# Kernel optimization log

Measured on AMD Instinct MI355X. Metric: run time of the kernel, lower is better.

The kernel has to match this reference:

```python
import jax, jax.numpy as jnp
import numpy as np

B, Q, KV = 2, 2048, 2048
D_MODEL = 1024
N_HEADS = 16
D_KV = 64
EPS = 1e-6


def setup_inputs() -> dict:
    key = jax.random.key(0)
    ks = jax.random.split(key, 7)
    s = 0.02
    return {
        "hidden_states": jax.random.normal(ks[0], (B, Q, D_MODEL), jnp.float32),
        "key_value_states": jax.random.normal(ks[1], (B, KV, D_MODEL), jnp.float32),
        "wq": jax.random.normal(ks[2], (D_MODEL, N_HEADS * D_KV), jnp.float32) * s,
        "wk": jax.random.normal(ks[3], (D_MODEL, N_HEADS * D_KV), jnp.float32) * s,
        "wv": jax.random.normal(ks[4], (D_MODEL, N_HEADS * D_KV), jnp.float32) * s,
        "wo": jax.random.normal(ks[5], (N_HEADS * D_KV, D_MODEL), jnp.float32) * s,
        "norm_w": jnp.ones((D_MODEL,), jnp.float32),
    }


def reference(hidden_states, key_value_states, wq, wk, wv, wo, norm_w):
    # RMSNorm (T5-style, no mean subtraction)
    var = jnp.mean(jnp.square(hidden_states), axis=-1, keepdims=True)
    normed = hidden_states * jax.lax.rsqrt(var + EPS) * norm_w

    b, q_len, _ = hidden_states.shape
    kv_len = key_value_states.shape[1]

    def split_heads(x):  # [b, s, H*d] -> [b, H, s, d]
        return x.reshape(b, -1, N_HEADS, D_KV).transpose(0, 2, 1, 3)

    q = split_heads(normed @ wq)              # [b,H,q,d]
    k = split_heads(key_value_states @ wk)    # [b,H,kv,d]
    v = split_heads(key_value_states @ wv)    # [b,H,kv,d]

    # T5 attention: NO 1/sqrt(d) scaling; position_bias is zeros here
    # (has_relative_attention_bias=False, no mask) so it is a no-op.
    scores = jnp.einsum("bhqd,bhkd->bhqk", q, k)
    attn = jax.nn.softmax(scores.astype(jnp.float32), axis=-1).astype(scores.dtype)
    ctx = jnp.einsum("bhqk,bhkd->bhqd", attn, v)
    ctx = ctx.transpose(0, 2, 1, 3).reshape(b, q_len, N_HEADS * D_KV)
    attn_out = ctx @ wo

    # residual connection
    return hidden_states + attn_out
```

## Files before the change

kernel.cpp:

```cpp
#include <hip/hip_runtime.h>


typedef __attribute__((ext_vector_type(8))) short  s16x8;
typedef __attribute__((ext_vector_type(4))) float  f32x4;
typedef __attribute__((ext_vector_type(4))) int    i32x4;

#define LOG2E 1.4426950408889634f
#define EXP2(x) __builtin_amdgcn_exp2f(x)

__device__ __forceinline__ unsigned short f2bf(float f) {
  unsigned int u = __builtin_bit_cast(unsigned int, f);
  return (unsigned short)((u + 0x7FFFu + ((u >> 16) & 1u)) >> 16);
}

__device__ __forceinline__ unsigned cvtpk(float lo, float hi) {
  unsigned r;
  asm("v_cvt_pk_bf16_f32 %0, %1, %2" : "=v"(r) : "v"(lo), "v"(hi));
  return r;
}

__device__ __forceinline__ void gload16(const void* g, void* l) {
  __builtin_amdgcn_global_load_lds(
      (const __attribute__((address_space(1))) unsigned int*)g,
      (__attribute__((address_space(3))) unsigned int*)l, 16, 0, 0);
}

__global__ __launch_bounds__(256) void k_transpose4(
    const float* __restrict__ a0, const float* __restrict__ a1,
    const float* __restrict__ a2, const float* __restrict__ a3,
    unsigned short* __restrict__ o0, unsigned short* __restrict__ o1,
    unsigned short* __restrict__ o2, unsigned short* __restrict__ o3) {
  int z = blockIdx.z;
  const float* in = (z == 0) ? a0 : (z == 1) ? a1 : (z == 2) ? a2 : a3;
  unsigned short* out = (z == 0) ? o0 : (z == 1) ? o1 : (z == 2) ? o2 : o3;
  __shared__ float tile[64][65];
  int t = threadIdx.x;
  int tx = t & 15, ty = t >> 4;
  int r0 = blockIdx.y * 64, c0 = blockIdx.x * 64;
#pragma unroll
  for (int p = 0; p < 4; ++p) {
    int r = p * 16 + ty;
    float4 v = *reinterpret_cast<const float4*>(in + (size_t)(r0 + r) * 1024 + c0 + tx * 4);
    tile[r][tx * 4 + 0] = v.x; tile[r][tx * 4 + 1] = v.y;
    tile[r][tx * 4 + 2] = v.z; tile[r][tx * 4 + 3] = v.w;
  }
  __syncthreads();
#pragma unroll
  for (int p = 0; p < 4; ++p) {
    int c = p * 16 + ty;
    unsigned int lo = (unsigned int)f2bf(tile[tx * 4 + 0][c]) |
                      ((unsigned int)f2bf(tile[tx * 4 + 1][c]) << 16);
    unsigned int hi = (unsigned int)f2bf(tile[tx * 4 + 2][c]) |
                      ((unsigned int)f2bf(tile[tx * 4 + 3][c]) << 16);
    uint2 pk2; pk2.x = lo; pk2.y = hi;
    *reinterpret_cast<uint2*>(out + (size_t)(c0 + c) * 1024 + r0 + tx * 4) = pk2;
  }
}

__global__ __launch_bounds__(256) void k_rmsnorm(
    const float* __restrict__ hs, const float* __restrict__ w,
    unsigned short* __restrict__ out) {
  int row = blockIdx.x, t = threadIdx.x;
  float4 v = *reinterpret_cast<const float4*>(hs + (size_t)row * 1024 + t * 4);
  float s = v.x * v.x + v.y * v.y + v.z * v.z + v.w * v.w;
#pragma unroll
  for (int m = 1; m < 64; m <<= 1) s += __shfl_xor(s, m);
  __shared__ float ps[4];
  if ((t & 63) == 0) ps[t >> 6] = s;
  __syncthreads();
  float tot = ps[0] + ps[1] + ps[2] + ps[3];
  float sc = rsqrtf(tot * (1.0f / 1024.0f) + 1e-6f) * LOG2E;
  float4 wv = *reinterpret_cast<const float4*>(w + t * 4);
  unsigned int lo = (unsigned int)f2bf(v.x * sc * wv.x) |
                    ((unsigned int)f2bf(v.y * sc * wv.y) << 16);
  unsigned int hi = (unsigned int)f2bf(v.z * sc * wv.z) |
                    ((unsigned int)f2bf(v.w * sc * wv.w) << 16);
  uint2 pk2; pk2.x = lo; pk2.y = hi;
  *reinterpret_cast<uint2*>(out + (size_t)row * 1024 + t * 4) = pk2;
}

__global__ __launch_bounds__(256) void k_cast(
    const float* __restrict__ in, unsigned short* __restrict__ out, int n4) {
  int i = blockIdx.x * 256 + threadIdx.x;
  int stride = gridDim.x * 256;
  for (; i < n4; i += stride) {
    float4 v = *reinterpret_cast<const float4*>(in + (size_t)i * 4);
    unsigned int lo = (unsigned int)f2bf(v.x) | ((unsigned int)f2bf(v.y) << 16);
    unsigned int hi = (unsigned int)f2bf(v.z) | ((unsigned int)f2bf(v.w) << 16);
    uint2 pk2; pk2.x = lo; pk2.y = hi;
    *reinterpret_cast<uint2*>(out + (size_t)i * 4) = pk2;
  }
}

__device__ __forceinline__ void gemm_body(
    const unsigned short* __restrict__ A, const unsigned short* __restrict__ Bt,
    void* __restrict__ Cout, const float* __restrict__ resid, int mode) {
  __shared__ __align__(16) char sm[65536];
  int t = threadIdx.x;
  int bn = blockIdx.x, bm = blockIdx.y;
  int m0 = bm * 128, n0 = bn * 128;
  int lane = t & 63, w = t >> 6, lr = lane & 15, lg = lane >> 4;
  int wr = w >> 1, wc = w & 1;

  f32x4 acc[4][4] = {};

  const char* aA = (const char*)A + ((size_t)(m0 + (t >> 3)) * 1024 + (t & 7) * 8) * 2;
  const char* aB = (const char*)Bt + ((size_t)(n0 + (t >> 3)) * 1024 + (t & 7) * 8) * 2;

  auto stage = [&](int buf, int kt) {
    int koff = kt * 128;
    char* As = sm + buf * 16384;
    char* Bs = sm + 32768 + buf * 16384;
#pragma unroll
    for (int c = 0; c < 4; ++c) {
      gload16(aA + (size_t)c * 65536 + koff, As + c * 4096 + t * 16);
      gload16(aB + (size_t)c * 65536 + koff, Bs + c * 4096 + t * 16);
    }
  };

  stage(0, 0);
  __syncthreads();
  int cur = 0;
  for (int kt = 0; kt < 16; ++kt) {
    if (kt < 15) stage(cur ^ 1, kt + 1);
    const char* As = sm + cur * 16384;
    const char* Bs = sm + 32768 + cur * 16384;
    s16x8 af[2][4], bfr[2][4];
#pragma unroll
    for (int ks = 0; ks < 2; ++ks) {
#pragma unroll
      for (int m = 0; m < 4; ++m)
        af[ks][m] = *reinterpret_cast<const s16x8*>(
            As + (wr * 64 + m * 16 + lr) * 128 + ks * 64 + lg * 16);
#pragma unroll
      for (int n = 0; n < 4; ++n)
        bfr[ks][n] = *reinterpret_cast<const s16x8*>(
            Bs + (wc * 64 + n * 16 + lr) * 128 + ks * 64 + lg * 16);
    }
#pragma unroll
    for (int ks = 0; ks < 2; ++ks)
#pragma unroll
      for (int m = 0; m < 4; ++m)
#pragma unroll
        for (int n = 0; n < 4; ++n)
          acc[m][n] = __builtin_amdgcn_mfma_f32_16x16x32_bf16(af[ks][m], bfr[ks][n], acc[m][n], 0, 0, 0);
    __syncthreads();
    cur ^= 1;
  }

#pragma unroll
  for (int m = 0; m < 4; ++m)
#pragma unroll
    for (int n = 0; n < 4; ++n) {
      int colg = n0 + wc * 64 + n * 16 + lr;
      int rowb = m0 + wr * 64 + m * 16 + lg * 4;
      if (mode == 0) {
        unsigned short* C = (unsigned short*)Cout;
#pragma unroll
        for (int r = 0; r < 4; ++r)
          C[(size_t)(rowb + r) * 1024 + colg] = f2bf(acc[m][n][r]);
      } else if (mode == 1) {
        int h = colg >> 6, d = colg & 63;
        int b = rowb >> 11, kv = rowb & 2047;
        unsigned short* C = (unsigned short*)Cout +
            ((size_t)((b * 16 + h) * 64 + d) * 2048 + kv);
        unsigned int lo = (unsigned int)f2bf(acc[m][n][0]) |
                          ((unsigned int)f2bf(acc[m][n][1]) << 16);
        unsigned int hi = (unsigned int)f2bf(acc[m][n][2]) |
                          ((unsigned int)f2bf(acc[m][n][3]) << 16);
        uint2 pk2; pk2.x = lo; pk2.y = hi;
        *reinterpret_cast<uint2*>(C) = pk2;
      } else {
        float* C = (float*)Cout;
#pragma unroll
        for (int r = 0; r < 4; ++r) {
          size_t idx = (size_t)(rowb + r) * 1024 + colg;
          C[idx] = resid[idx] + acc[m][n][r];
        }
      }
    }
}

__global__ __launch_bounds__(256) void k_gemm_qkv(
    const unsigned short* __restrict__ normed, const unsigned short* __restrict__ kvb,
    const unsigned short* __restrict__ wqT, const unsigned short* __restrict__ wkT,
    const unsigned short* __restrict__ wvT,
    unsigned short* __restrict__ qb, unsigned short* __restrict__ kb,
    unsigned short* __restrict__ vTb) {
  int z = blockIdx.z;
  const unsigned short* A = (z == 0) ? normed : kvb;
  const unsigned short* B = (z == 0) ? wqT : (z == 1) ? wkT : wvT;
  void* C = (z == 0) ? (void*)qb : (z == 1) ? (void*)kb : (void*)vTb;
  gemm_body(A, B, C, nullptr, (z == 2) ? 1 : 0);
}

__global__ __launch_bounds__(256) void k_gemm_o(
    const unsigned short* __restrict__ ctxb, const unsigned short* __restrict__ woT,
    float* __restrict__ out, const float* __restrict__ hs) {
  gemm_body(ctxb, woT, (void*)out, hs, 2);
}

__global__ __launch_bounds__(512, 4) void k_attn(
    const unsigned short* __restrict__ q, const unsigned short* __restrict__ k,
    const unsigned short* __restrict__ vt, unsigned short* __restrict__ ctx) {
  __shared__ __align__(16) char sm[65536];
  int t = threadIdx.x, w = t >> 6, lane = t & 63, lr = lane & 15, lg = lane >> 4;

  int bid = blockIdx.x;
  int xcd = bid & 7, slot = bid >> 3;
  int bh = xcd * 4 + (slot >> 4);
  int qt = slot & 15;
  int b = bh >> 4, h = bh & 15;

  const char* qB = (const char*)q + ((size_t)(b * 2048 + qt * 128) * 1024 + h * 64) * 2;
  const char* kB = (const char*)k + ((size_t)(b * 2048) * 1024 + h * 64) * 2;
  const char* vB = (const char*)vt + (size_t)bh * 64 * 4096;

  int krow = t >> 3;
  int kcb  = ((t & 7) * 16) ^ ((krow & 7) << 4);
  int vrow = t >> 4;
  int vcb  = ((t & 15) * 16) ^ ((vrow & 7) << 4);

  auto stageKV = [&](int buf, int it2) {
    char* Kd = sm + buf * 16384;
    char* Vd = sm + 32768 + buf * 16384;
    const char* kb2 = kB + (size_t)(it2 * 128) * 2048;
    const char* vb2 = vB + it2 * 256;
#pragma unroll
    for (int c = 0; c < 2; ++c) {
      gload16(kb2 + (size_t)(c * 64 + krow) * 2048 + kcb, Kd + c * 8192 + t * 16);
      gload16(vb2 + (size_t)(c * 32 + vrow) * 4096 + vcb, Vd + c * 8192 + t * 16);
    }
  };

#pragma unroll
  for (int c = 0; c < 2; ++c)
    gload16(qB + (size_t)(c * 64 + krow) * 2048 + kcb, sm + c * 8192 + t * 16);
  __syncthreads();
  s16x8 qa[2];
#pragma unroll
  for (int ks = 0; ks < 2; ++ks) {
    int row = w * 16 + lr;
    qa[ks] = *reinterpret_cast<const s16x8*>(
        sm + row * 128 + ((ks * 64 + lg * 16) ^ ((lr & 7) << 4)));
  }
  __syncthreads();
  stageKV(0, 0);
  asm volatile("s_waitcnt vmcnt(0)" ::: "memory");
  __builtin_amdgcn_s_barrier();
  __builtin_amdgcn_sched_barrier(0);

  f32x4 octx[4] = {};
  float mrun = -1e30f;
  float lsum = 0.0f;

  int cur = 0;
  for (int it = 0; it < 16; ++it) {
    if (it < 15) stageKV(cur ^ 1, it + 1);

    const char* Ks = sm + cur * 16384;
    const char* Vs = sm + 32768 + cur * 16384;

    f32x4 s2[8] = {};
#pragma unroll
    for (int ks = 0; ks < 2; ++ks) {
      s16x8 ka[8];
#pragma unroll
      for (int n = 0; n < 8; ++n)
        ka[n] = *reinterpret_cast<const s16x8*>(
            Ks + (n * 16 + lr) * 128 + ((ks * 64 + lg * 16) ^ ((lr & 7) << 4)));
#pragma unroll
      for (int n = 0; n < 8; ++n)
        s2[n] = __builtin_amdgcn_mfma_f32_16x16x32_bf16(ka[n], qa[ks], s2[n], 0, 0, 0);
    }

    float m2 = s2[0][0];
#pragma unroll
    for (int n = 0; n < 8; ++n)
#pragma unroll
      for (int r = 0; r < 4; ++r) m2 = fmaxf(m2, s2[n][r]);
    m2 = fmaxf(m2, __shfl_xor(m2, 16));
    m2 = fmaxf(m2, __shfl_xor(m2, 32));
    if (__any(m2 > mrun + 8.0f)) {
      float mx = fmaxf(mrun, m2);
      float sc = EXP2(mrun - mx);
      mrun = mx;
      lsum *= sc;
#pragma unroll
      for (int r = 0; r < 4; ++r) {
        float scr = __shfl(sc, lg * 4 + r);
#pragma unroll
        for (int nd = 0; nd < 4; ++nd) octx[nd][r] *= scr;
      }
    }

    unsigned pk[8][2];
    {
      float a0 = 0.0f, a1 = 0.0f, a2 = 0.0f, a3 = 0.0f;
#pragma unroll
      for (int n = 0; n < 8; ++n) {
        float p0 = EXP2(s2[n][0] - mrun);
        float p1 = EXP2(s2[n][1] - mrun);
        float p2 = EXP2(s2[n][2] - mrun);
        float p3 = EXP2(s2[n][3] - mrun);
        a0 += p0; a1 += p1; a2 += p2; a3 += p3;
        pk[n][0] = cvtpk(p0, p1);
        pk[n][1] = cvtpk(p2, p3);
      }
      lsum += (a0 + a1) + (a2 + a3);
    }

#pragma unroll
    for (int ks = 0; ks < 4; ++ks) {
      s16x8 vb[4];
#pragma unroll
      for (int nd = 0; nd < 4; ++nd) {
        int row = nd * 16 + lr;
        int swz = (lr & 7) << 4;
        uint2 v1 = *reinterpret_cast<const uint2*>(
            Vs + row * 256 + ((ks * 64 + lg * 8) ^ swz));
        uint2 v2 = *reinterpret_cast<const uint2*>(
            Vs + row * 256 + ((ks * 64 + 32 + lg * 8) ^ swz));
        i32x4 vv; vv[0] = (int)v1.x; vv[1] = (int)v1.y;
        vv[2] = (int)v2.x; vv[3] = (int)v2.y;
        vb[nd] = __builtin_bit_cast(s16x8, vv);
      }
      i32x4 pv;
      pv[0] = (int)pk[2 * ks][0];     pv[1] = (int)pk[2 * ks][1];
      pv[2] = (int)pk[2 * ks + 1][0]; pv[3] = (int)pk[2 * ks + 1][1];
      s16x8 pa = __builtin_bit_cast(s16x8, pv);
#pragma unroll
      for (int nd = 0; nd < 4; ++nd)
        octx[nd] = __builtin_amdgcn_mfma_f32_16x16x32_bf16(pa, vb[nd], octx[nd], 0, 0, 0);
    }

    if (it < 15) {
      asm volatile("s_waitcnt vmcnt(0)" ::: "memory");
      __builtin_amdgcn_s_barrier();
      __builtin_amdgcn_sched_barrier(0);
      cur ^= 1;
    }
  }

  {
    float tot = lsum;
    tot += __shfl_xor(tot, 16);
    tot += __shfl_xor(tot, 32);
    float inv = 1.0f / tot;
#pragma unroll
    for (int r = 0; r < 4; ++r) {
      float invr = __shfl(inv, lg * 4 + r);
      int qrow = qt * 128 + w * 16 + lg * 4 + r;
#pragma unroll
      for (int nd = 0; nd < 4; ++nd)
        ctx[(size_t)(b * 2048 + qrow) * 1024 + h * 64 + nd * 16 + lr] =
            f2bf(octx[nd][r] * invr);
    }
  }
}

extern "C" void kernel_launch(void* const* d_in, const int* in_sizes, int n_in,
                              void* d_out, int out_size, void* d_ws, size_t ws_size,
                              hipStream_t stream) {
  const float* hs  = (const float*)d_in[0];
  const float* kvs = (const float*)d_in[1];
  const float* wq  = (const float*)d_in[2];
  const float* wk  = (const float*)d_in[3];
  const float* wv  = (const float*)d_in[4];
  const float* wo  = (const float*)d_in[5];
  const float* nw  = (const float*)d_in[6];
  float* out = (float*)d_out;
  char* ws = (char*)d_ws;

  unsigned short* normed = (unsigned short*)(ws + (size_t)0);
  unsigned short* kvb    = (unsigned short*)(ws + ((size_t)8 << 20));
  unsigned short* wqT    = (unsigned short*)(ws + ((size_t)16 << 20));
  unsigned short* wkT    = (unsigned short*)(ws + ((size_t)18 << 20));
  unsigned short* wvT    = (unsigned short*)(ws + ((size_t)20 << 20));
  unsigned short* woT    = (unsigned short*)(ws + ((size_t)22 << 20));
  unsigned short* qb     = (unsigned short*)(ws + ((size_t)24 << 20));
  unsigned short* kb     = (unsigned short*)(ws + ((size_t)32 << 20));
  unsigned short* vTb    = (unsigned short*)(ws + ((size_t)40 << 20));
  unsigned short* ctxb   = (unsigned short*)(ws + ((size_t)48 << 20));

  k_transpose4<<<dim3(16, 16, 4), 256, 0, stream>>>(wq, wk, wv, wo, wqT, wkT, wvT, woT);
  k_rmsnorm<<<4096, 256, 0, stream>>>(hs, nw, normed);
  k_cast<<<1024, 256, 0, stream>>>(kvs, kvb, 1048576);

  k_gemm_qkv<<<dim3(8, 32, 3), 256, 0, stream>>>(normed, kvb, wqT, wkT, wvT, qb, kb, vTb);

  k_attn<<<512, 512, 0, stream>>>(qb, kb, vTb, ctxb);

  k_gemm_o<<<dim3(8, 32), 256, 0, stream>>>(ctxb, woT, out, hs);
}
```

Before: 141.9 us.

## Prefetch attention KV two tiles ahead, fuse prep kernels, shrink O-proj tile

The attention loop now keeps two K/V tiles in flight and waits only for the older one with a partial vmcnt. It also raises wave priority around the MFMA blocks and uses three-input max for the row max. The RMSNorm and bf16 cast kernels are merged into one launch. The GEMM body is templated on M tile and mode, so the output projection uses 64-row tiles to double its block count. The aims are to hide load latency, cut launch overhead and improve occupancy on the small O GEMM, at the risk of a wrong vmcnt count if the per-stage load count differs.

Result: slower. 169.9 us (+19.7%).

```diff
diff --git a/kernel.cpp b/kernel.cpp
--- a/kernel.cpp
+++ b/kernel.cpp
@@ -17,6 +17,10 @@
   unsigned r;
   asm("v_cvt_pk_bf16_f32 %0, %1, %2" : "=v"(r) : "v"(lo), "v"(hi));
   return r;
+}
+
+__device__ __forceinline__ float f3max(float a, float b, float c) {
+  return fmaxf(fmaxf(a, b), c);
 }
 
 __device__ __forceinline__ void gload16(const void* g, void* l) {
@@ -57,65 +61,69 @@
   }
 }
 
-__global__ __launch_bounds__(256) void k_rmsnorm(
+__global__ __launch_bounds__(256) void k_prep(
     const float* __restrict__ hs, const float* __restrict__ w,
-    unsigned short* __restrict__ out) {
-  int row = blockIdx.x, t = threadIdx.x;
-  float4 v = *reinterpret_cast<const float4*>(hs + (size_t)row * 1024 + t * 4);
-  float s = v.x * v.x + v.y * v.y + v.z * v.z + v.w * v.w;
-#pragma unroll
-  for (int m = 1; m < 64; m <<= 1) s += __shfl_xor(s, m);
-  __shared__ float ps[4];
-  if ((t & 63) == 0) ps[t >> 6] = s;
-  __syncthreads();
-  float tot = ps[0] + ps[1] + ps[2] + ps[3];
-  float sc = rsqrtf(tot * (1.0f / 1024.0f) + 1e-6f) * LOG2E;
-  float4 wv = *reinterpret_cast<const float4*>(w + t * 4);
-  unsigned int lo = (unsigned int)f2bf(v.x * sc * wv.x) |
-                    ((unsigned int)f2bf(v.y * sc * wv.y) << 16);
-  unsigned int hi = (unsigned int)f2bf(v.z * sc * wv.z) |
-                    ((unsigned int)f2bf(v.w * sc * wv.w) << 16);
-  uint2 pk2; pk2.x = lo; pk2.y = hi;
-  *reinterpret_cast<uint2*>(out + (size_t)row * 1024 + t * 4) = pk2;
-}
-
-__global__ __launch_bounds__(256) void k_cast(
-    const float* __restrict__ in, unsigned short* __restrict__ out, int n4) {
-  int i = blockIdx.x * 256 + threadIdx.x;
-  int stride = gridDim.x * 256;
-  for (; i < n4; i += stride) {
-    float4 v = *reinterpret_cast<const float4*>(in + (size_t)i * 4);
-    unsigned int lo = (unsigned int)f2bf(v.x) | ((unsigned int)f2bf(v.y) << 16);
-    unsigned int hi = (unsigned int)f2bf(v.z) | ((unsigned int)f2bf(v.w) << 16);
+    unsigned short* __restrict__ normed,
+    const float* __restrict__ kvs, unsigned short* __restrict__ kvb) {
+  int t = threadIdx.x;
+  if (blockIdx.x < 4096) {
+    int row = blockIdx.x;
+    float4 v = *reinterpret_cast<const float4*>(hs + (size_t)row * 1024 + t * 4);
+    float s = v.x * v.x + v.y * v.y + v.z * v.z + v.w * v.w;
+#pragma unroll
+    for (int m = 1; m < 64; m <<= 1) s += __shfl_xor(s, m);
+    __shared__ float ps[4];
+    if ((t & 63) == 0) ps[t >> 6] = s;
+    __syncthreads();
+    float tot = ps[0] + ps[1] + ps[2] + ps[3];
+    float sc = rsqrtf(tot * (1.0f / 1024.0f) + 1e-6f) * LOG2E;
+    float4 wv = *reinterpret_cast<const float4*>(w + t * 4);
+    unsigned int lo = (unsigned int)f2bf(v.x * sc * wv.x) |
+                      ((unsigned int)f2bf(v.y * sc * wv.y) << 16);
+    unsigned int hi = (unsigned int)f2bf(v.z * sc * wv.z) |
+                      ((unsigned int)f2bf(v.w * sc * wv.w) << 16);
     uint2 pk2; pk2.x = lo; pk2.y = hi;
-    *reinterpret_cast<uint2*>(out + (size_t)i * 4) = pk2;
-  }
-}
-
+    *reinterpret_cast<uint2*>(normed + (size_t)row * 1024 + t * 4) = pk2;
+  } else {
+    int i = (blockIdx.x - 4096) * 256 + t;
+    for (; i < 1048576; i += 1024 * 256) {
+      float4 v = *reinterpret_cast<const float4*>(kvs + (size_t)i * 4);
+      unsigned int lo = (unsigned int)f2bf(v.x) | ((unsigned int)f2bf(v.y) << 16);
+      unsigned int hi = (unsigned int)f2bf(v.z) | ((unsigned int)f2bf(v.w) << 16);
+      uint2 pk2; pk2.x = lo; pk2.y = hi;
+      *reinterpret_cast<uint2*>(kvb + (size_t)i * 4) = pk2;
+    }
+  }
+}
+
+template <int BM, int MODE>
 __device__ __forceinline__ void gemm_body(
     const unsigned short* __restrict__ A, const unsigned short* __restrict__ Bt,
-    void* __restrict__ Cout, const float* __restrict__ resid, int mode) {
-  __shared__ __align__(16) char sm[65536];
+    void* __restrict__ Cout, const float* __restrict__ resid) {
+  constexpr int MF = BM / 32;
+  constexpr int ATILE = BM * 128;
+  __shared__ __align__(16) char sm[2 * ATILE + 32768];
   int t = threadIdx.x;
   int bn = blockIdx.x, bm = blockIdx.y;
-  int m0 = bm * 128, n0 = bn * 128;
+  int m0 = bm * BM, n0 = bn * 128;
   int lane = t & 63, w = t >> 6, lr = lane & 15, lg = lane >> 4;
   int wr = w >> 1, wc = w & 1;
 
-  f32x4 acc[4][4] = {};
+  f32x4 acc[MF][4] = {};
 
   const char* aA = (const char*)A + ((size_t)(m0 + (t >> 3)) * 1024 + (t & 7) * 8) * 2;
   const char* aB = (const char*)Bt + ((size_t)(n0 + (t >> 3)) * 1024 + (t & 7) * 8) * 2;
 
   auto stage = [&](int buf, int kt) {
     int koff = kt * 128;
-    char* As = sm + buf * 16384;
-    char* Bs = sm + 32768 + buf * 16384;
-#pragma unroll
-    for (int c = 0; c < 4; ++c) {
+    char* As = sm + buf * ATILE;
+    char* Bs = sm + 2 * ATILE + buf * 16384;
+#pragma unroll
+    for (int c = 0; c < BM / 32; ++c)
       gload16(aA + (size_t)c * 65536 + koff, As + c * 4096 + t * 16);
+#pragma unroll
+    for (int c = 0; c < 4; ++c)
       gload16(aB + (size_t)c * 65536 + koff, Bs + c * 4096 + t * 16);
-    }
   };
 
   stage(0, 0);
@@ -123,15 +131,15 @@
   int cur = 0;
   for (int kt = 0; kt < 16; ++kt) {
     if (kt < 15) stage(cur ^ 1, kt + 1);
-    const char* As = sm + cur * 16384;
-    const char* Bs = sm + 32768 + cur * 16384;
-    s16x8 af[2][4], bfr[2][4];
+    const char* As = sm + cur * ATILE;
+    const char* Bs = sm + 2 * ATILE + cur * 16384;
+    s16x8 af[2][MF], bfr[2][4];
 #pragma unroll
     for (int ks = 0; ks < 2; ++ks) {
 #pragma unroll
-      for (int m = 0; m < 4; ++m)
+      for (int m = 0; m < MF; ++m)
         af[ks][m] = *reinterpret_cast<const s16x8*>(
-            As + (wr * 64 + m * 16 + lr) * 128 + ks * 64 + lg * 16);
+            As + (wr * (BM / 2) + m * 16 + lr) * 128 + ks * 64 + lg * 16);
 #pragma unroll
       for (int n = 0; n < 4; ++n)
         bfr[ks][n] = *reinterpret_cast<const s16x8*>(
@@ -140,7 +148,7 @@
 #pragma unroll
     for (int ks = 0; ks < 2; ++ks)
 #pragma unroll
-      for (int m = 0; m < 4; ++m)
+      for (int m = 0; m < MF; ++m)
 #pragma unroll
         for (int n = 0; n < 4; ++n)
           acc[m][n] = __builtin_amdgcn_mfma_f32_16x16x32_bf16(af[ks][m], bfr[ks][n], acc[m][n], 0, 0, 0);
@@ -149,17 +157,17 @@
   }
 
 #pragma unroll
-  for (int m = 0; m < 4; ++m)
+  for (int m = 0; m < MF; ++m)
 #pragma unroll
     for (int n = 0; n < 4; ++n) {
       int colg = n0 + wc * 64 + n * 16 + lr;
-      int rowb = m0 + wr * 64 + m * 16 + lg * 4;
-      if (mode == 0) {
+      int rowb = m0 + wr * (BM / 2) + m * 16 + lg * 4;
+      if (MODE == 0) {
         unsigned short* C = (unsigned short*)Cout;
 #pragma unroll
         for (int r = 0; r < 4; ++r)
           C[(size_t)(rowb + r) * 1024 + colg] = f2bf(acc[m][n][r]);
-      } else if (mode == 1) {
+      } else if (MODE == 1) {
         int h = colg >> 6, d = colg & 63;
         int b = rowb >> 11, kv = rowb & 2047;
         unsigned short* C = (unsigned short*)Cout +
@@ -190,14 +198,18 @@
   int z = blockIdx.z;
   const unsigned short* A = (z == 0) ? normed : kvb;
   const unsigned short* B = (z == 0) ? wqT : (z == 1) ? wkT : wvT;
-  void* C = (z == 0) ? (void*)qb : (z == 1) ? (void*)kb : (void*)vTb;
-  gemm_body(A, B, C, nullptr, (z == 2) ? 1 : 0);
+  if (z == 2)
+    gemm_body<128, 1>(A, B, (void*)vTb, nullptr);
+  else if (z == 1)
+    gemm_body<128, 0>(A, B, (void*)kb, nullptr);
+  else
+    gemm_body<128, 0>(A, B, (void*)qb, nullptr);
 }
 
 __global__ __launch_bounds__(256) void k_gemm_o(
     const unsigned short* __restrict__ ctxb, const unsigned short* __restrict__ woT,
     float* __restrict__ out, const float* __restrict__ hs) {
-  gemm_body(ctxb, woT, (void*)out, hs, 2);
+  gemm_body<64, 2>(ctxb, woT, (void*)out, hs);
 }
 
 __global__ __launch_bounds__(512, 4) void k_attn(
@@ -246,22 +258,26 @@
   }
   __syncthreads();
   stageKV(0, 0);
-  asm volatile("s_waitcnt vmcnt(0)" ::: "memory");
-  __builtin_amdgcn_s_barrier();
-  __builtin_amdgcn_sched_barrier(0);
+  stageKV(1, 1);
 
   f32x4 octx[4] = {};
   float mrun = -1e30f;
   float lsum = 0.0f;
 
-  int cur = 0;
   for (int it = 0; it < 16; ++it) {
-    if (it < 15) stageKV(cur ^ 1, it + 1);
-
-    const char* Ks = sm + cur * 16384;
-    const char* Vs = sm + 32768 + cur * 16384;
+    if (it < 14) {
+      asm volatile("s_waitcnt vmcnt(4)" ::: "memory");
+    } else {
+      asm volatile("s_waitcnt vmcnt(0)" ::: "memory");
+    }
+    __builtin_amdgcn_s_barrier();
+    __builtin_amdgcn_sched_barrier(0);
+
+    const char* Ks = sm + (it & 1) * 16384;
+    const char* Vs = sm + 32768 + (it & 1) * 16384;
 
     f32x4 s2[8] = {};
+    __builtin_amdgcn_s_setprio(1);
 #pragma unroll
     for (int ks = 0; ks < 2; ++ks) {
       s16x8 ka[8];
@@ -273,12 +289,12 @@
       for (int n = 0; n < 8; ++n)
         s2[n] = __builtin_amdgcn_mfma_f32_16x16x32_bf16(ka[n], qa[ks], s2[n], 0, 0, 0);
     }
-
-    float m2 = s2[0][0];
+    __builtin_amdgcn_s_setprio(0);
+
+    float m2 = -1e30f;
 #pragma unroll
     for (int n = 0; n < 8; ++n)
-#pragma unroll
-      for (int r = 0; r < 4; ++r) m2 = fmaxf(m2, s2[n][r]);
+      m2 = f3max(f3max(m2, s2[n][0], s2[n][1]), s2[n][2], s2[n][3]);
     m2 = fmaxf(m2, __shfl_xor(m2, 16));
     m2 = fmaxf(m2, __shfl_xor(m2, 32));
     if (__any(m2 > mrun + 8.0f)) {
@@ -310,6 +326,7 @@
       lsum += (a0 + a1) + (a2 + a3);
     }
 
+    __builtin_amdgcn_s_setprio(1);
 #pragma unroll
     for (int ks = 0; ks < 4; ++ks) {
       s16x8 vb[4];
@@ -333,13 +350,11 @@
       for (int nd = 0; nd < 4; ++nd)
         octx[nd] = __builtin_amdgcn_mfma_f32_16x16x32_bf16(pa, vb[nd], octx[nd], 0, 0, 0);
     }
-
-    if (it < 15) {
-      asm volatile("s_waitcnt vmcnt(0)" ::: "memory");
-      __builtin_amdgcn_s_barrier();
-      __builtin_amdgcn_sched_barrier(0);
-      cur ^= 1;
-    }
+    __builtin_amdgcn_s_setprio(0);
+
+    __builtin_amdgcn_s_barrier();
+    __builtin_amdgcn_sched_barrier(0);
+    if (it < 14) stageKV(it & 1, it + 2);
   }
 
   {
@@ -384,12 +399,11 @@
   unsigned short* ctxb   = (unsigned short*)(ws + ((size_t)48 << 20));
 
   k_transpose4<<<dim3(16, 16, 4), 256, 0, stream>>>(wq, wk, wv, wo, wqT, wkT, wvT, woT);
-  k_rmsnorm<<<4096, 256, 0, stream>>>(hs, nw, normed);
-  k_cast<<<1024, 256, 0, stream>>>(kvs, kvb, 1048576);
+  k_prep<<<5120, 256, 0, stream>>>(hs, nw, normed, kvs, kvb);
 
   k_gemm_qkv<<<dim3(8, 32, 3), 256, 0, stream>>>(normed, kvb, wqT, wkT, wvT, qb, kb, vTb);
 
   k_attn<<<512, 512, 0, stream>>>(qb, kb, vTb, ctxb);
 
-  k_gemm_o<<<dim3(8, 32), 256, 0, stream>>>(ctxb, woT, out, hs);
-}
+  k_gemm_o<<<dim3(8, 64), 256, 0, stream>>>(ctxb, woT, out, hs);
+}
```
